# Optimization experiments

Hardware: AMD Instinct MI355X
Metric: run time of the kernel (lower is better)

Reference implementation:

```python
import jax, jax.numpy as jnp
import numpy as np

B, C, E, S, L, N = 2, 256, 256, 3, 5, 128
HMAX = 128
LEVEL_SIZES = np.array([128, 64, 32, 16, 8])
STRIDES = np.array([8.0, 16.0, 32.0, 64.0, 128.0])
GROUPS = 8
EPS = 1e-5


def setup_inputs() -> dict:
    key = jax.random.key(0)
    ks = jax.random.split(key, 16)
    # Padded FPN pyramid stacked as [L, B, C, HMAX, HMAX]; level l valid in [:sz, :sz]
    fm = jnp.zeros((L, B, C, HMAX, HMAX), jnp.float32)
    for l in range(L):
        sz = int(LEVEL_SIZES[l])
        fm = fm.at[l, :, :, :sz, :sz].set(jax.random.normal(ks[l], (B, C, sz, sz), jnp.float32))
    # Boxes in 1024x1024 image coordinates (x1, y1, x2, y2)
    cxy = jax.random.uniform(ks[5], (N, 2), minval=60.0, maxval=960.0)
    wh = jax.random.uniform(ks[6], (N, 2), minval=8.0, maxval=96.0)
    boxes = jnp.concatenate([cxy - wh / 2, cxy + wh / 2], axis=1)
    batch_idx = jax.random.randint(ks[7], (N,), 0, B, jnp.int32)
    level_idx = jax.random.randint(ks[8], (N,), 0, L, jnp.int32)
    sym_ids = jax.random.randint(ks[9], (N,), 0, 6, jnp.int32)
    conv_w = jax.random.normal(ks[10], (E, C, 3, 3), jnp.float32) / np.float32(np.sqrt(C * 9))
    gn_scale = jnp.ones((E,), jnp.float32)
    gn_bias = jnp.zeros((E,), jnp.float32)
    head_w = jax.random.normal(ks[11], (E, E), jnp.float32) / np.float32(np.sqrt(E))
    head_b = jnp.zeros((E,), jnp.float32)
    spat_w = jax.random.normal(ks[12], (E, 4), jnp.float32) * 0.01
    spat_b = jnp.zeros((E,), jnp.float32)
    sym_emb = jax.random.normal(ks[13], (6, E), jnp.float32) * 0.05
    fuse_w = jax.random.normal(ks[14], (6, E, E), jnp.float32) / np.float32(np.sqrt(E))
    fuse_b = jnp.zeros((6, E), jnp.float32)
    return dict(feature_maps=fm, boxes=boxes, conv_w=conv_w, gn_scale=gn_scale,
                gn_bias=gn_bias, head_w=head_w, head_b=head_b, spat_w=spat_w,
                spat_b=spat_b, sym_emb=sym_emb, fuse_w=fuse_w, fuse_b=fuse_b,
                batch_idx=batch_idx, level_idx=level_idx, sym_ids=sym_ids)


def _roi_align(fm, boxes, batch_idx, level_idx):
    # Batched roi_align (aligned=False, sampling_ratio=1) over all boxes at once.
    scale = (1.0 / jnp.asarray(STRIDES, fm.dtype))[level_idx]          # [N]
    hv = jnp.asarray(LEVEL_SIZES, fm.dtype)[level_idx]                 # [N] valid H=W per box
    x1 = boxes[:, 0] * scale; y1 = boxes[:, 1] * scale
    x2 = boxes[:, 2] * scale; y2 = boxes[:, 3] * scale
    roi_w = jnp.maximum(x2 - x1, 1.0)
    roi_h = jnp.maximum(y2 - y1, 1.0)
    off = (jnp.arange(S, dtype=fm.dtype) + 0.5) / S                    # bin centers
    xs = x1[:, None] + off[None, :] * roi_w[:, None]                   # [N,S]
    ys = y1[:, None] + off[None, :] * roi_h[:, None]                   # [N,S]
    y = jnp.broadcast_to(ys[:, :, None], (ys.shape[0], S, S))          # [N,S,S]
    x = jnp.broadcast_to(xs[:, None, :], (xs.shape[0], S, S))
    hvb = hv[:, None, None]
    valid = (y > -1.0) & (y < hvb) & (x > -1.0) & (x < hvb)
    yc = jnp.clip(y, 0.0, hvb - 1.0)
    xc = jnp.clip(x, 0.0, hvb - 1.0)
    y0 = jnp.floor(yc).astype(jnp.int32)
    x0 = jnp.floor(xc).astype(jnp.int32)
    hi = (hvb - 1.0).astype(jnp.int32)
    y1i = jnp.minimum(y0 + 1, hi)
    x1i = jnp.minimum(x0 + 1, hi)
    ly = yc - y0.astype(fm.dtype)
    lx = xc - x0.astype(fm.dtype)
    lvl = level_idx[:, None, None]
    bix = batch_idx[:, None, None]

    def g(yi, xi):
        # gather only the 4 corner pixels -> [N,S,S,C]
        return fm[lvl, bix, :, yi, xi]

    v = ((1 - ly) * (1 - lx))[..., None] * g(y0, x0) \
      + ((1 - ly) * lx)[..., None] * g(y0, x1i) \
      + (ly * (1 - lx))[..., None] * g(y1i, x0) \
      + (ly * lx)[..., None] * g(y1i, x1i)
    v = jnp.where(valid[..., None], v, 0.0)
    return jnp.transpose(v, (0, 3, 1, 2))                              # [N,C,S,S]


def _forward(feature_maps, boxes, conv_w, gn_scale, gn_bias, head_w, head_b,
             spat_w, spat_b, sym_emb, fuse_w, fuse_b, batch_idx, level_idx, sym_ids):
    roi = _roi_align(feature_maps, boxes, batch_idx, level_idx)        # [N,C,S,S]
    h = jax.lax.conv_general_dilated(roi, conv_w, (1, 1), ((1, 1), (1, 1)),
                                     dimension_numbers=('NCHW', 'OIHW', 'NCHW'))  # [N,E,S,S]
    n = h.shape[0]
    hg = h.reshape(n, GROUPS, -1)
    mu = hg.mean(-1, keepdims=True)
    var = hg.var(-1, keepdims=True)
    hg = (hg - mu) * jax.lax.rsqrt(var + EPS)
    h = hg.reshape(h.shape) * gn_scale[None, :, None, None] + gn_bias[None, :, None, None]
    h = jax.nn.relu(h)
    h = h.reshape(n, E, -1).mean(-1)                                   # spatial mean -> [N,E]
    head_out = jax.nn.relu(h @ head_w.T + head_b)                      # sym_feat_nn + ReLU
    spat = jax.nn.relu(boxes @ spat_w.T + spat_b)                      # spatial_embeddings
    fused_in = head_out + spat + sym_emb[sym_ids]                      # + class embedding
    out = jax.nn.relu(jnp.einsum('ne,nfe->nf', fused_in, fuse_w[sym_ids]) + fuse_b[sym_ids])
    return out                                                          # [N,E]


def reference(feature_maps, boxes, conv_w, gn_scale, gn_bias, head_w, head_b,
              spat_w, spat_b, sym_emb, fuse_w, fuse_b, batch_idx, level_idx, sym_ids):
    return _forward(feature_maps, boxes, conv_w, gn_scale, gn_bias, head_w, head_b,
                    spat_w, spat_b, sym_emb, fuse_w, fuse_b, batch_idx, level_idx, sym_ids)
```

## Files before the change

kernel.cpp:

```cpp
#include <hip/hip_runtime.h>
#include <hip/hip_bf16.h>


typedef float v2f __attribute__((ext_vector_type(2)));

__device__ __forceinline__ float bf_lo(unsigned u) { return __uint_as_float(u << 16); }
__device__ __forceinline__ float bf_hi(unsigned u) { return __uint_as_float(u & 0xffff0000u); }
__device__ __forceinline__ unsigned short f2bf(float f) {
    __hip_bfloat16 h = __float2bfloat16(f);
    return *(unsigned short*)&h;
}

__global__ __launch_bounds__(256) void prep_k(
    const float* __restrict__ conv_w,
    const float* __restrict__ head_w, const float* __restrict__ fuse_w,
    const float* __restrict__ fm, const float* __restrict__ boxes,
    const int* __restrict__ batch_idx, const int* __restrict__ level_idx,
    unsigned short* __restrict__ w8, unsigned short* __restrict__ w9,
    unsigned short* __restrict__ head_wTb, unsigned short* __restrict__ fuse_wTb,
    float* __restrict__ roiT) {
    int blk = blockIdx.x;
    int t = threadIdx.x;

    if (blk < 256) {
        int c = blk, e = t;
        const float* src = conv_w + ((size_t)e * 256 + c) * 9;
        unsigned short tmp[8];
#pragma unroll
        for (int k = 0; k < 8; ++k) tmp[k] = f2bf(src[k]);
        ((uint4*)w8)[(size_t)c * 256 + e] = *(const uint4*)tmp;
        w9[(size_t)c * 256 + e] = f2bf(src[8]);
        return;
    }

    if (blk < 704) {
        __shared__ float tile[32][33];
        int q = blk - 256;
        int z = q >> 6;
        int rem = q & 63;
        int bx = (rem & 7) * 32, by = (rem >> 3) * 32;
        const float* in = (z == 0) ? head_w : fuse_w + (size_t)(z - 1) * 65536;
        unsigned short* out = (z == 0) ? head_wTb : fuse_wTb + (size_t)(z - 1) * 65536;
        int tx = t & 31, ty = t >> 5;
#pragma unroll
        for (int i = 0; i < 32; i += 8)
            tile[ty + i][tx] = in[(size_t)(by + ty + i) * 256 + bx + tx];
        __syncthreads();
#pragma unroll
        for (int i = 0; i < 32; i += 8) {
            int k = bx + ty + i;
            int e = by + tx;
            out[(size_t)((k >> 1) * 256 + e) * 2 + (k & 1)] = f2bf(tile[tx][ty + i]);
        }
        return;
    }

    {
        int c = blk - 704;
        int n = t & 127;
        int p0 = t >> 7;

        int lvl = level_idx[n];
        int b = batch_idx[n];
        const float sizes[5]  = {128.f, 64.f, 32.f, 16.f, 8.f};
        const float invstr[5] = {1.f/8.f, 1.f/16.f, 1.f/32.f, 1.f/64.f, 1.f/128.f};
        float scale = invstr[lvl];
        float hv = sizes[lvl];

        float x1 = boxes[n*4+0] * scale, y1 = boxes[n*4+1] * scale;
        float x2 = boxes[n*4+2] * scale, y2 = boxes[n*4+3] * scale;
        float rw = fmaxf(x2 - x1, 1.f), rh = fmaxf(y2 - y1, 1.f);
        int hi = (int)(hv - 1.f);

        const float* base = fm + (((size_t)lvl * 2 + b) * 256 + c) * (128 * 128);

        for (int p = p0; p < 9; p += 2) {
            int i = p / 3, j = p % 3;
            float x = x1 + (((float)j + 0.5f) / 3.f) * rw;
            float y = y1 + (((float)i + 0.5f) / 3.f) * rh;

            bool valid = (y > -1.f) && (y < hv) && (x > -1.f) && (x < hv);
            float yc = fminf(fmaxf(y, 0.f), hv - 1.f);
            float xc = fminf(fmaxf(x, 0.f), hv - 1.f);
            int y0 = (int)floorf(yc), x0 = (int)floorf(xc);
            int y1i = min(y0 + 1, hi), x1i = min(x0 + 1, hi);
            float ly = yc - (float)y0, lx = xc - (float)x0;

            float v00 = base[y0 * 128 + x0];
            float v01 = base[y0 * 128 + x1i];
            float v10 = base[y1i * 128 + x0];
            float v11 = base[y1i * 128 + x1i];
            float v = (1.f - ly) * (1.f - lx) * v00 + (1.f - ly) * lx * v01 +
                      ly * (1.f - lx) * v10 + ly * lx * v11;
            roiT[((size_t)n * 9 + p) * 256 + c] = valid ? v : 0.f;
        }
    }
}

__global__ __launch_bounds__(512, 2) void conv_gn_pool(
    const float* __restrict__ roiT,
    const unsigned short* __restrict__ w8, const unsigned short* __restrict__ w9,
    const float* __restrict__ gn_scale, const float* __restrict__ gn_bias,
    float* __restrict__ pooled) {
    __shared__ float redA[4 * 64 * 9];
    __shared__ float redB[4 * 64 * 9];

    int np = blockIdx.x >> 2;
    int eq = blockIdx.x & 3;
    int n0 = np * 2, n1 = n0 + 1;
    int t = threadIdx.x;
    int e_loc = t & 63;
    int ch = __builtin_amdgcn_readfirstlane(t >> 6);
    int e = eq * 64 + e_loc;

    const float* r0 = roiT + (size_t)n0 * 2304;
    const float* r1 = roiT + (size_t)n1 * 2304;

    v2f acc[9];
#pragma unroll
    for (int p = 0; p < 9; ++p) acc[p] = (v2f)(0.f);

    int c0 = ch * 32;
#pragma unroll 2
    for (int c = c0; c < c0 + 32; c += 2) {
        v2f q0[9], q1[9];
#pragma unroll
        for (int jj = 0; jj < 9; ++jj) {
            q0[jj] = *(const v2f*)(r0 + jj * 256 + c);
            q1[jj] = *(const v2f*)(r1 + jj * 256 + c);
        }
        v2f rc0[9], rc1[9];
#pragma unroll
        for (int jj = 0; jj < 9; ++jj) {
            rc0[jj].x = q0[jj].x; rc0[jj].y = q1[jj].x;
            rc1[jj].x = q0[jj].y; rc1[jj].y = q1[jj].y;
        }
#pragma unroll
        for (int cc = 0; cc < 2; ++cc) {
            const v2f* r = cc ? rc1 : rc0;
            int cw = c + cc;
            uint4 wa4 = ((const uint4*)w8)[(size_t)cw * 256 + e];
            float wv[9];
            wv[0] = bf_lo(wa4.x); wv[1] = bf_hi(wa4.x);
            wv[2] = bf_lo(wa4.y); wv[3] = bf_hi(wa4.y);
            wv[4] = bf_lo(wa4.z); wv[5] = bf_hi(wa4.z);
            wv[6] = bf_lo(wa4.w); wv[7] = bf_hi(wa4.w);
            wv[8] = bf_lo((unsigned)w9[(size_t)cw * 256 + e]);
#pragma unroll
            for (int ky = 0; ky < 3; ++ky) {
#pragma unroll
                for (int kx = 0; kx < 3; ++kx) {
                    v2f w2;
                    w2.x = wv[ky * 3 + kx]; w2.y = wv[ky * 3 + kx];
#pragma unroll
                    for (int oy = 0; oy < 3; ++oy) {
                        int iy = oy + ky - 1;
                        if (iy < 0 || iy > 2) continue;
#pragma unroll
                        for (int ox = 0; ox < 3; ++ox) {
                            int ix = ox + kx - 1;
                            if (ix < 0 || ix > 2) continue;
                            int o = oy * 3 + ox, in = iy * 3 + ix;
                            acc[o] = w2 * r[in] + acc[o];
                        }
                    }
                }
            }
        }
    }

    float acc0[9], acc1[9];
#pragma unroll
    for (int p = 0; p < 9; ++p) { acc0[p] = acc[p].x; acc1[p] = acc[p].y; }

    if (ch >= 4) {
#pragma unroll
        for (int p = 0; p < 9; ++p) {
            redA[((ch - 4) * 64 + e_loc) * 9 + p] = acc0[p];
            redB[((ch - 4) * 64 + e_loc) * 9 + p] = acc1[p];
        }
    }
    __syncthreads();
    if (ch < 4) {
#pragma unroll
        for (int p = 0; p < 9; ++p) {
            acc0[p] += redA[(ch * 64 + e_loc) * 9 + p];
            acc1[p] += redB[(ch * 64 + e_loc) * 9 + p];
        }
    }
    __syncthreads();
    if (ch >= 2 && ch < 4) {
#pragma unroll
        for (int p = 0; p < 9; ++p) {
            redA[((ch - 2) * 64 + e_loc) * 9 + p] = acc0[p];
            redB[((ch - 2) * 64 + e_loc) * 9 + p] = acc1[p];
        }
    }
    __syncthreads();
    if (ch < 2) {
#pragma unroll
        for (int p = 0; p < 9; ++p) {
            acc0[p] += redA[(ch * 64 + e_loc) * 9 + p];
            acc1[p] += redB[(ch * 64 + e_loc) * 9 + p];
        }
    }
    __syncthreads();
    if (ch == 1) {
#pragma unroll
        for (int p = 0; p < 9; ++p) redA[e_loc * 9 + p] = acc0[p];
    }
    if (ch == 0) {
#pragma unroll
        for (int p = 0; p < 9; ++p) redB[e_loc * 9 + p] = acc1[p];
    }
    __syncthreads();

    if (ch < 2) {
        float accf[9];
        int n_out;
        if (ch == 0) {
            n_out = n0;
#pragma unroll
            for (int p = 0; p < 9; ++p) accf[p] = acc0[p] + redA[e_loc * 9 + p];
        } else {
            n_out = n1;
#pragma unroll
            for (int p = 0; p < 9; ++p) accf[p] = acc1[p] + redB[e_loc * 9 + p];
        }

        float s = 0.f, sq = 0.f;
#pragma unroll
        for (int p = 0; p < 9; ++p) { s += accf[p]; sq += accf[p] * accf[p]; }
#pragma unroll
        for (int m = 16; m >= 1; m >>= 1) {
            s  += __shfl_xor(s, m, 64);
            sq += __shfl_xor(sq, m, 64);
        }
        float mean = s * (1.f / 288.f);
        float var = sq * (1.f / 288.f) - mean * mean;
        float rinv = rsqrtf(var + 1e-5f);
        float gs = gn_scale[e], gb = gn_bias[e];
        float ps = 0.f;
#pragma unroll
        for (int p = 0; p < 9; ++p) {
            float v = (accf[p] - mean) * rinv * gs + gb;
            ps += fmaxf(v, 0.f);
        }
        pooled[(size_t)n_out * 256 + e] = ps * (1.f / 9.f);
    }
}

__global__ __launch_bounds__(512) void head_fuse(
    const float* __restrict__ pooled, const float* __restrict__ boxes,
    const unsigned short* __restrict__ head_wTb, const float* __restrict__ head_b,
    const float* __restrict__ spat_w, const float* __restrict__ spat_b,
    const float* __restrict__ sym_emb,
    const unsigned short* __restrict__ fuse_wTb, const float* __restrict__ fuse_b,
    const int* __restrict__ sym_ids, float* __restrict__ out) {
    __shared__ float pl[256];
    __shared__ float part[512];
    __shared__ float fin[256];
    int n = blockIdx.x;
    int t = threadIdx.x;
    int e = t & 255;
    int kh = t >> 8;
    int sid = sym_ids[n];

    if (t < 256) pl[t] = pooled[(size_t)n * 256 + t];
    __syncthreads();

    {
        float acc = 0.f;
        const unsigned* w = (const unsigned*)head_wTb + (size_t)(kh * 64) * 256 + e;
        const float* p = pl + kh * 128;
#pragma unroll 8
        for (int kp = 0; kp < 64; ++kp) {
            unsigned u = w[kp * 256];
            acc = fmaf(p[2 * kp],     bf_lo(u), acc);
            acc = fmaf(p[2 * kp + 1], bf_hi(u), acc);
        }
        part[t] = acc;
    }
    __syncthreads();
    if (t < 256) {
        float ho = fmaxf(part[t] + part[t + 256] + head_b[t], 0.f);
        float4 sw = ((const float4*)spat_w)[t];
        float b0 = boxes[n*4+0], b1 = boxes[n*4+1], b2 = boxes[n*4+2], b3 = boxes[n*4+3];
        float sp = fmaxf(spat_b[t] + b0*sw.x + b1*sw.y + b2*sw.z + b3*sw.w, 0.f);
        fin[t] = ho + sp + sym_emb[sid * 256 + t];
    }
    __syncthreads();
    {
        float o = 0.f;
        const unsigned* w = (const unsigned*)fuse_wTb + (size_t)sid * 32768
                            + (size_t)(kh * 64) * 256 + e;
        const float* p = fin + kh * 128;
#pragma unroll 8
        for (int kp = 0; kp < 64; ++kp) {
            unsigned u = w[kp * 256];
            o = fmaf(p[2 * kp],     bf_lo(u), o);
            o = fmaf(p[2 * kp + 1], bf_hi(u), o);
        }
        part[t] = o;
    }
    __syncthreads();
    if (t < 256)
        out[(size_t)n * 256 + t] = fmaxf(part[t] + part[t + 256] + fuse_b[sid * 256 + t], 0.f);
}

extern "C" void kernel_launch(void* const* d_in, const int* in_sizes, int n_in,
                              void* d_out, int out_size, void* d_ws, size_t ws_size,
                              hipStream_t stream) {
    const float* fm      = (const float*)d_in[0];
    const float* boxes   = (const float*)d_in[1];
    const float* conv_w  = (const float*)d_in[2];
    const float* gn_s    = (const float*)d_in[3];
    const float* gn_b    = (const float*)d_in[4];
    const float* head_w  = (const float*)d_in[5];
    const float* head_b  = (const float*)d_in[6];
    const float* spat_w  = (const float*)d_in[7];
    const float* spat_b  = (const float*)d_in[8];
    const float* sym_emb = (const float*)d_in[9];
    const float* fuse_w  = (const float*)d_in[10];
    const float* fuse_b  = (const float*)d_in[11];
    const int* batch_idx = (const int*)d_in[12];
    const int* level_idx = (const int*)d_in[13];
    const int* sym_ids   = (const int*)d_in[14];
    float* outp = (float*)d_out;

    char* ws = (char*)d_ws;
    unsigned short* w8       = (unsigned short*)ws;
    unsigned short* w9       = (unsigned short*)(ws + 1048576);
    unsigned short* head_wTb = (unsigned short*)(ws + 1179648);
    unsigned short* fuse_wTb = (unsigned short*)(ws + 1310720);
    float* roiT    = (float*)(ws + 2097152);
    float* pooled  = (float*)(ws + 3276800);

    prep_k<<<960, 256, 0, stream>>>(conv_w, head_w, fuse_w, fm, boxes,
                                    batch_idx, level_idx,
                                    w8, w9, head_wTb, fuse_wTb, roiT);
    conv_gn_pool<<<256, 512, 0, stream>>>(roiT, w8, w9, gn_s, gn_b, pooled);
    head_fuse<<<128, 512, 0, stream>>>(pooled, boxes, head_wTb, head_b, spat_w, spat_b,
                                       sym_emb, fuse_wTb, fuse_b, sym_ids, outp);
}
```

Measured before the change: 251.0 us.

## Fuse ROI-align sampling into conv kernel via shared memory

Moves the bilinear ROI-align sampling out of the prep kernel and into the conv/GN/pool kernel. Each block samples its two boxes' 9x256 values straight into shared memory, removing the roiT global round-trip and shrinking the prep launch. Block indexing is reordered so blocks that share a box pair are spread across the grid. The cost is that each of the 4 e-quarter blocks per box pair repeats the same gather from the feature maps, and the kernel uses more LDS.

Result: no change. 253.8 us (+1.1%).

```diff
diff --git a/kernel.cpp b/kernel.cpp
--- a/kernel.cpp
+++ b/kernel.cpp
@@ -14,11 +14,8 @@
 __global__ __launch_bounds__(256) void prep_k(
     const float* __restrict__ conv_w,
     const float* __restrict__ head_w, const float* __restrict__ fuse_w,
-    const float* __restrict__ fm, const float* __restrict__ boxes,
-    const int* __restrict__ batch_idx, const int* __restrict__ level_idx,
     unsigned short* __restrict__ w8, unsigned short* __restrict__ w9,
-    unsigned short* __restrict__ head_wTb, unsigned short* __restrict__ fuse_wTb,
-    float* __restrict__ roiT) {
+    unsigned short* __restrict__ head_wTb, unsigned short* __restrict__ fuse_wTb) {
     int blk = blockIdx.x;
     int t = threadIdx.x;
 
@@ -33,7 +30,7 @@
         return;
     }
 
-    if (blk < 704) {
+    {
         __shared__ float tile[32][33];
         int q = blk - 256;
         int z = q >> 6;
@@ -52,13 +49,31 @@
             int e = by + tx;
             out[(size_t)((k >> 1) * 256 + e) * 2 + (k & 1)] = f2bf(tile[tx][ty + i]);
         }
-        return;
-    }
+    }
+}
+
+__global__ __launch_bounds__(512, 2) void conv_gn_pool(
+    const float* __restrict__ fm, const float* __restrict__ boxes,
+    const int* __restrict__ batch_idx, const int* __restrict__ level_idx,
+    const unsigned short* __restrict__ w8, const unsigned short* __restrict__ w9,
+    const float* __restrict__ gn_scale, const float* __restrict__ gn_bias,
+    float* __restrict__ pooled) {
+    __shared__ float roiA[9 * 256];
+    __shared__ float roiB[9 * 256];
+    __shared__ float redA[4 * 64 * 9];
+    __shared__ float redB[4 * 64 * 9];
+
+    int blk = blockIdx.x;
+    int np = blk & 63;
+    int eq = blk >> 6;
+    int n0 = np * 2, n1 = n0 + 1;
+    int t = threadIdx.x;
 
     {
-        int c = blk - 704;
-        int n = t & 127;
-        int p0 = t >> 7;
+        int c = t & 255;
+        int half = t >> 8;
+        int n = half ? n1 : n0;
+        float* dst = half ? roiB : roiA;
 
         int lvl = level_idx[n];
         int b = batch_idx[n];
@@ -74,7 +89,8 @@
 
         const float* base = fm + (((size_t)lvl * 2 + b) * 256 + c) * (128 * 128);
 
-        for (int p = p0; p < 9; p += 2) {
+#pragma unroll
+        for (int p = 0; p < 9; ++p) {
             int i = p / 3, j = p % 3;
             float x = x1 + (((float)j + 0.5f) / 3.f) * rw;
             float y = y1 + (((float)i + 0.5f) / 3.f) * rh;
@@ -92,29 +108,17 @@
             float v11 = base[y1i * 128 + x1i];
             float v = (1.f - ly) * (1.f - lx) * v00 + (1.f - ly) * lx * v01 +
                       ly * (1.f - lx) * v10 + ly * lx * v11;
-            roiT[((size_t)n * 9 + p) * 256 + c] = valid ? v : 0.f;
-        }
-    }
-}
-
-__global__ __launch_bounds__(512, 2) void conv_gn_pool(
-    const float* __restrict__ roiT,
-    const unsigned short* __restrict__ w8, const unsigned short* __restrict__ w9,
-    const float* __restrict__ gn_scale, const float* __restrict__ gn_bias,
-    float* __restrict__ pooled) {
-    __shared__ float redA[4 * 64 * 9];
-    __shared__ float redB[4 * 64 * 9];
-
-    int np = blockIdx.x >> 2;
-    int eq = blockIdx.x & 3;
-    int n0 = np * 2, n1 = n0 + 1;
-    int t = threadIdx.x;
+            dst[p * 256 + c] = valid ? v : 0.f;
+        }
+    }
+    __syncthreads();
+
     int e_loc = t & 63;
     int ch = __builtin_amdgcn_readfirstlane(t >> 6);
     int e = eq * 64 + e_loc;
 
-    const float* r0 = roiT + (size_t)n0 * 2304;
-    const float* r1 = roiT + (size_t)n1 * 2304;
+    const float* r0 = roiA;
+    const float* r1 = roiB;
 
     v2f acc[9];
 #pragma unroll
@@ -333,13 +337,12 @@
     unsigned short* w9       = (unsigned short*)(ws + 1048576);
     unsigned short* head_wTb = (unsigned short*)(ws + 1179648);
     unsigned short* fuse_wTb = (unsigned short*)(ws + 1310720);
-    float* roiT    = (float*)(ws + 2097152);
-    float* pooled  = (float*)(ws + 3276800);
-
-    prep_k<<<960, 256, 0, stream>>>(conv_w, head_w, fuse_w, fm, boxes,
-                                    batch_idx, level_idx,
-                                    w8, w9, head_wTb, fuse_wTb, roiT);
-    conv_gn_pool<<<256, 512, 0, stream>>>(roiT, w8, w9, gn_s, gn_b, pooled);
+    float* pooled  = (float*)(ws + 2097152);
+
+    prep_k<<<704, 256, 0, stream>>>(conv_w, head_w, fuse_w,
+                                    w8, w9, head_wTb, fuse_wTb);
+    conv_gn_pool<<<256, 512, 0, stream>>>(fm, boxes, batch_idx, level_idx,
+                                          w8, w9, gn_s, gn_b, pooled);
     head_fuse<<<128, 512, 0, stream>>>(pooled, boxes, head_wTb, head_b, spat_w, spat_b,
                                        sym_emb, fuse_wTb, fuse_b, sym_ids, outp);
 }
```
